# Kernel optimization log

Hardware: AMD Instinct MI355X
Metric: run time of the kernel (lower is better)

Reference implementation:

```python
import jax, jax.numpy as jnp
import numpy as np

B, D, H, NB = 16384, 1024, 256, 16

def setup_inputs() -> dict:
    key = jax.random.key(0)
    ks = jax.random.split(key, 10)
    s_d = 1.0 / np.sqrt(D)
    s_h = 1.0 / np.sqrt(H)
    return {
        "x":   jax.random.normal(ks[0], (B, D), jnp.float32),
        # switch: Linear(D,H) -> relu -> Linear(H, 3*NB)
        "Ws1": jax.random.normal(ks[1], (D, H), jnp.float32) * s_d,
        "bs1": jnp.zeros((H,), jnp.float32),
        "Ws2": jax.random.normal(ks[2], (H, 3 * NB), jnp.float32) * s_h,
        "bs2": jnp.zeros((3 * NB,), jnp.float32),
        # per-branch bottleneck FC operators: D -> H -> D
        "W1":  jax.random.normal(ks[3], (NB, D, H), jnp.float32) * s_d,
        "b1":  jnp.zeros((NB, H), jnp.float32),
        "W2":  jax.random.normal(ks[4], (NB, H, D), jnp.float32) * s_h,
        "b2":  jnp.zeros((NB, D), jnp.float32),
        # noise: uniform for gumbel, normal for reparameterized gaussian
        "u":   jax.random.uniform(ks[5], (B, NB), jnp.float32, 1e-6, 1.0 - 1e-6),
        "eps": jax.random.normal(ks[6], (B, NB), jnp.float32),
    }

def reference(x, Ws1, bs1, Ws2, bs2, W1, b1, W2, b2, u, eps):
    # switch -> control signals, reshaped to (B, 3, NB)
    ctrl = jax.nn.relu(x @ Ws1 + bs1) @ Ws2 + bs2
    ctrl = ctrl.reshape(-1, 3, NB)
    y_logits, z_mean, z_logvar = ctrl[:, 0], ctrl[:, 1], ctrl[:, 2]

    # gumbel-softmax sample (tau = 1)
    g = -jnp.log(-jnp.log(u))
    y = jax.nn.softmax(y_logits + g, axis=-1)          # soft sample (B, NB)
    y_idx = jnp.argmax(y, axis=-1)                     # hard branch per sample

    # gaussian reparameterization
    z = z_mean + jnp.exp(0.5 * z_logvar) * eps         # (B, NB)

    # per-branch bottleneck FC, z of the branch gates the bottleneck
    h = jax.nn.relu(jnp.einsum('bd,ndh->bnh', x, W1) + b1)   # (B, NB, H)
    h = h * z[:, :, None]
    o = jnp.einsum('bnh,nhd->bnd', h, W2) + b2               # (B, NB, D)

    # combine: keep only the branch selected by y_idx
    onehot = jax.nn.one_hot(y_idx, NB, dtype=x.dtype)        # (B, NB)
    out = jnp.einsum('bnd,bn->bd', o, onehot)                # (B, D)

    return (x + out, y_logits, y_idx, y, z_mean, z_logvar, z)
```

## Files before the change

### kernel.cpp

```cpp
#include <hip/hip_runtime.h>
#include <hip/hip_bf16.h>
#include <stdint.h>

#define Bn 16384
#define Dd 1024
#define Hh 256
#define NBk 16

#define O1 ((size_t)Bn*Dd)
#define O2 (O1 + (size_t)Bn*NBk)
#define O3 (O2 + (size_t)Bn)
#define O4 (O3 + (size_t)Bn*NBk)
#define O5 (O4 + (size_t)Bn*NBk)
#define O6 (O5 + (size_t)Bn*NBk)

typedef __attribute__((ext_vector_type(8))) short s16x8;
typedef __attribute__((ext_vector_type(4))) float f32x4;

#define MFMA_BF16(a,b,c) __builtin_amdgcn_mfma_f32_16x16x32_bf16((a),(b),(c),0,0,0)

__device__ __forceinline__ float blo(unsigned v){ return __uint_as_float(v << 16); }
__device__ __forceinline__ float bhi(unsigned v){ return __uint_as_float(v & 0xFFFF0000u); }
__device__ __forceinline__ unsigned short f2b(float f){
  unsigned u = __float_as_uint(f);
  return (unsigned short)((u + 0x7FFFu + ((u >> 16) & 1u)) >> 16);
}
__device__ __forceinline__ s16x8 cvt8(const f32x4 u0, const f32x4 u1) {
  s16x8 v;
  v[0]=(short)f2b(u0[0]); v[1]=(short)f2b(u0[1]); v[2]=(short)f2b(u0[2]); v[3]=(short)f2b(u0[3]);
  v[4]=(short)f2b(u1[0]); v[5]=(short)f2b(u1[1]); v[6]=(short)f2b(u1[2]); v[7]=(short)f2b(u1[3]);
  return v;
}
__device__ __forceinline__ void split8(const f32x4 u0, const f32x4 u1, s16x8& hi, s16x8& lo) {
  #pragma unroll
  for (int e = 0; e < 4; ++e) {
    const unsigned short h = f2b(u0[e]);
    hi[e] = (short)h;
    lo[e] = (short)f2b(u0[e] - __uint_as_float((unsigned)h << 16));
  }
  #pragma unroll
  for (int e = 0; e < 4; ++e) {
    const unsigned short h = f2b(u1[e]);
    hi[4+e] = (short)h;
    lo[4+e] = (short)f2b(u1[e] - __uint_as_float((unsigned)h << 16));
  }
}
__device__ __forceinline__ void gload16(const void* g, void* lds) {
  __builtin_amdgcn_global_load_lds(
      (const __attribute__((address_space(1))) unsigned int*)g,
      (__attribute__((address_space(3))) unsigned int*)lds, 16, 0, 0);
}

__global__ __launch_bounds__(256) void kA1(const float* __restrict__ x, const float* __restrict__ Ws1,
                                           const float* __restrict__ bs1, float* __restrict__ A1)
{
  const int b0 = blockIdx.x * 64;
  const int c0 = blockIdx.y * 128;
  __shared__ float XS[32][68];
  __shared__ float WS[32][128];
  const int tid = threadIdx.x;
  const int ty = tid >> 4, tx = tid & 15;
  float acc[4][8];
  #pragma unroll
  for (int r = 0; r < 4; ++r)
    #pragma unroll
    for (int c = 0; c < 8; ++c) acc[r][c] = 0.f;

  for (int k0 = 0; k0 < Dd; k0 += 32) {
    #pragma unroll
    for (int it = 0; it < 2; ++it) {
      int i = tid + 256*it;
      int row = i >> 3, kq = i & 7;
      float4 v = *(const float4*)&x[(size_t)(b0+row)*Dd + k0 + 4*kq];
      XS[4*kq+0][row] = v.x; XS[4*kq+1][row] = v.y; XS[4*kq+2][row] = v.z; XS[4*kq+3][row] = v.w;
    }
    #pragma unroll
    for (int it = 0; it < 4; ++it) {
      int i = tid + 256*it;
      int k = i >> 5, cq = i & 31;
      *(float4*)&WS[k][4*cq] = *(const float4*)&Ws1[(size_t)(k0+k)*Hh + c0 + 4*cq];
    }
    __syncthreads();
    #pragma unroll
    for (int k = 0; k < 32; ++k) {
      const float4 xv = *(const float4*)&XS[k][ty*4];
      const float4 w0 = *(const float4*)&WS[k][tx*4];
      const float4 w1 = *(const float4*)&WS[k][tx*4+64];
      const float xr[4] = {xv.x, xv.y, xv.z, xv.w};
      const float wr[8] = {w0.x,w0.y,w0.z,w0.w,w1.x,w1.y,w1.z,w1.w};
      #pragma unroll
      for (int r = 0; r < 4; ++r)
        #pragma unroll
        for (int c = 0; c < 8; ++c)
          acc[r][c] = fmaf(xr[r], wr[c], acc[r][c]);
    }
    __syncthreads();
  }
  const float4 bv0 = *(const float4*)&bs1[c0 + tx*4];
  const float4 bv1 = *(const float4*)&bs1[c0 + tx*4 + 64];
  const float br[8] = {bv0.x,bv0.y,bv0.z,bv0.w,bv1.x,bv1.y,bv1.z,bv1.w};
  #pragma unroll
  for (int r = 0; r < 4; ++r) {
    int row = b0 + ty*4 + r;
    float o[8];
    #pragma unroll
    for (int c = 0; c < 8; ++c) o[c] = fmaxf(acc[r][c] + br[c], 0.f);
    float4 s0 = {o[0],o[1],o[2],o[3]};
    float4 s1 = {o[4],o[5],o[6],o[7]};
    *(float4*)&A1[(size_t)row*Hh + c0 + tx*4]      = s0;
    *(float4*)&A1[(size_t)row*Hh + c0 + tx*4 + 64] = s1;
  }
}

__global__ __launch_bounds__(256) void kTW(const float* __restrict__ in,
                                           unsigned short* __restrict__ hi,
                                           unsigned short* __restrict__ lo)
{
  const int i0 = blockIdx.x * 32, j0 = blockIdx.y * 32;
  __shared__ float T[32][33];
  const int t = threadIdx.x;
  {
    const int ii = t >> 3, jj = (t & 7) * 4;
    float4 v = *(const float4*)&in[(size_t)(i0+ii)*Hh + j0 + jj];
    T[ii][jj] = v.x; T[ii][jj+1] = v.y; T[ii][jj+2] = v.z; T[ii][jj+3] = v.w;
  }
  __syncthreads();
  {
    const int jo = t >> 3, io = (t & 7) * 4;
    ushort4 sh, sl;
    float v0 = T[io+0][jo], v1 = T[io+1][jo], v2 = T[io+2][jo], v3 = T[io+3][jo];
    unsigned short h;
    h = f2b(v0); sh.x = h; sl.x = f2b(v0 - __uint_as_float((unsigned)h << 16));
    h = f2b(v1); sh.y = h; sl.y = f2b(v1 - __uint_as_float((unsigned)h << 16));
    h = f2b(v2); sh.z = h; sl.z = f2b(v2 - __uint_as_float((unsigned)h << 16));
    h = f2b(v3); sh.w = h; sl.w = f2b(v3 - __uint_as_float((unsigned)h << 16));
    *(ushort4*)&hi[(size_t)(j0+jo)*Dd + i0 + io] = sh;
    *(ushort4*)&lo[(size_t)(j0+jo)*Dd + i0 + io] = sl;
  }
}

__global__ __launch_bounds__(256) void kT2(const float* __restrict__ Ws2, float* __restrict__ Ws2T)
{
  const int j = blockIdx.x;
  const int k = threadIdx.x;
  Ws2T[(size_t)j * Hh + k] = Ws2[(size_t)k * 48 + j];
}

__global__ __launch_bounds__(256) void kA1s3(const float* __restrict__ x,
    const unsigned short* __restrict__ Whi, const unsigned short* __restrict__ Wlo,
    const float* __restrict__ bs1, float* __restrict__ A1)
{
  __shared__ __align__(16) unsigned short Xh[32*64];
  __shared__ __align__(16) unsigned short Xl[32*64];
  __shared__ __align__(16) unsigned short Bh[128*64];
  __shared__ __align__(16) unsigned short Bl[128*64];

  const int bid = blockIdx.x;
  const int b0 = (bid >> 1) * 32;
  const int cb = bid & 1;
  const int tid = threadIdx.x, l = tid & 63, w = tid >> 6;

  const int xrow = tid >> 3, xga = tid & 7;
  const int xdst = xrow * 128 + (xga ^ (xrow & 7)) * 16;
  const size_t xsrc = (size_t)(b0 + xrow) * Dd + xga * 8;

  const unsigned short *hsrc[4], *lsrc[4];
  const unsigned short* Hbase = Whi + (size_t)(cb * 128) * Dd;
  const unsigned short* Lbase = Wlo + (size_t)(cb * 128) * Dd;
  #pragma unroll
  for (int t = 0; t < 4; ++t) {
    const int col = (w * 4 + t) * 8 + (l >> 3);
    const int sa = (l & 7) ^ (col & 7);
    hsrc[t] = Hbase + (size_t)col * Dd + sa * 8;
    lsrc[t] = Lbase + (size_t)col * Dd + sa * 8;
  }

  f32x4 acc[2][2];
  #pragma unroll
  for (int a = 0; a < 2; ++a)
    #pragma unroll
    for (int b_ = 0; b_ < 2; ++b_)
      #pragma unroll
      for (int e = 0; e < 4; ++e) acc[a][b_][e] = 0.f;

  f32x4 xa = *(const f32x4*)&x[xsrc];
  f32x4 xb = *(const f32x4*)&x[xsrc + 4];

  for (int kc = 0; kc < 16; ++kc) {
    #pragma unroll
    for (int t = 0; t < 4; ++t) {
      gload16(hsrc[t] + kc * 64, (char*)Bh + (w * 4 + t) * 1024);
      gload16(lsrc[t] + kc * 64, (char*)Bl + (w * 4 + t) * 1024);
    }
    {
      s16x8 hi8, lo8;
      split8(xa, xb, hi8, lo8);
      *(s16x8*)((char*)Xh + xdst) = hi8;
      *(s16x8*)((char*)Xl + xdst) = lo8;
    }
    __syncthreads();

    if (kc < 15) {
      xa = *(const f32x4*)&x[xsrc + (kc + 1) * 64];
      xb = *(const f32x4*)&x[xsrc + (kc + 1) * 64 + 4];
    }

    #pragma unroll
    for (int kk = 0; kk < 2; ++kk) {
      s16x8 ah[2], al[2], bh[2], bl[2];
      #pragma unroll
      for (int rf = 0; rf < 2; ++rf) {
        const int row = rf * 16 + (l & 15);
        const int g = (kk * 4 + (l >> 4)) ^ (row & 7);
        ah[rf] = *(const s16x8*)((const char*)Xh + row * 128 + g * 16);
        al[rf] = *(const s16x8*)((const char*)Xl + row * 128 + g * 16);
      }
      #pragma unroll
      for (int cf = 0; cf < 2; ++cf) {
        const int col = w * 32 + cf * 16 + (l & 15);
        const int g = (kk * 4 + (l >> 4)) ^ (col & 7);
        bh[cf] = *(const s16x8*)((const char*)Bh + col * 128 + g * 16);
        bl[cf] = *(const s16x8*)((const char*)Bl + col * 128 + g * 16);
      }
      #pragma unroll
      for (int rf = 0; rf < 2; ++rf)
        #pragma unroll
        for (int cf = 0; cf < 2; ++cf) {
          acc[rf][cf] = MFMA_BF16(ah[rf], bh[cf], acc[rf][cf]);
          acc[rf][cf] = MFMA_BF16(ah[rf], bl[cf], acc[rf][cf]);
          acc[rf][cf] = MFMA_BF16(al[rf], bh[cf], acc[rf][cf]);
        }
    }
    __syncthreads();
  }

  #pragma unroll
  for (int rf = 0; rf < 2; ++rf)
    #pragma unroll
    for (int cf = 0; cf < 2; ++cf)
      #pragma unroll
      for (int rg = 0; rg < 4; ++rg) {
        const int row = b0 + rf * 16 + (l >> 4) * 4 + rg;
        const int col = cb * 128 + w * 32 + cf * 16 + (l & 15);
        A1[(size_t)row * Hh + col] = fmaxf(acc[rf][cf][rg] + bs1[col], 0.f);
      }
}

__global__ __launch_bounds__(256) void kA2(const float* __restrict__ Ws2, const float* __restrict__ bs2,
                                           float* out)
{
  const int b0 = blockIdx.x * 64;
  __shared__ float XS[32][68];
  __shared__ float WC[32][48];
  const int tid = threadIdx.x;
  const int rg = tid >> 4, jg = tid & 15;
  float acc[4][3];
  #pragma unroll
  for (int r = 0; r < 4; ++r) { acc[r][0]=0.f; acc[r][1]=0.f; acc[r][2]=0.f; }
  const float* A1 = out;
  for (int kc = 0; kc < 8; ++kc) {
    const int k0 = kc*32;
    #pragma unroll
    for (int it = 0; it < 2; ++it) {
      int i = tid + 256*it;
      int row = i >> 3, kq = i & 7;
      float4 v = *(const float4*)&A1[(size_t)(b0+row)*Hh + k0 + 4*kq];
      XS[4*kq+0][row]=v.x; XS[4*kq+1][row]=v.y; XS[4*kq+2][row]=v.z; XS[4*kq+3][row]=v.w;
    }
    #pragma unroll
    for (int it = 0; it < 2; ++it) {
      int i = tid + 256*it;
      if (i < 384) {
        int k = i / 12, jq = i % 12;
        *(float4*)&WC[k][4*jq] = *(const float4*)&Ws2[(size_t)(k0+k)*48 + 4*jq];
      }
    }
    __syncthreads();
    #pragma unroll
    for (int k = 0; k < 32; ++k) {
      const float4 av = *(const float4*)&XS[k][rg*4];
      const float ar[4] = {av.x,av.y,av.z,av.w};
      const float w0 = WC[k][jg], w1 = WC[k][jg+16], w2 = WC[k][jg+32];
      #pragma unroll
      for (int r = 0; r < 4; ++r) {
        acc[r][0] = fmaf(ar[r], w0, acc[r][0]);
        acc[r][1] = fmaf(ar[r], w1, acc[r][1]);
        acc[r][2] = fmaf(ar[r], w2, acc[r][2]);
      }
    }
    __syncthreads();
  }
  const float c0b = bs2[jg], c1b = bs2[jg+16], c2b = bs2[jg+32];
  #pragma unroll
  for (int r = 0; r < 4; ++r) {
    size_t row = (size_t)b0 + rg*4 + r;
    out[O1 + row*NBk + jg] = acc[r][0] + c0b;
    out[O4 + row*NBk + jg] = acc[r][1] + c1b;
    out[O5 + row*NBk + jg] = acc[r][2] + c2b;
  }
}

__global__ __launch_bounds__(256) void kB2(const float* __restrict__ u, const float* __restrict__ eps,
                                           float* out, int* __restrict__ idxw, float* __restrict__ zsel,
                                           int* __restrict__ counts)
{
  const int e = blockIdx.x * 256 + threadIdx.x;
  const int b = e >> 4, j = e & 15;
  const float yl = out[O1 + e];
  const float zm = out[O4 + e];
  const float zv = out[O5 + e];
  const float s  = yl - logf(-logf(u[e]));
  const float z  = zm + expf(0.5f * zv) * eps[e];

  float bv = s; int bj = j;
  #pragma unroll
  for (int m = 8; m >= 1; m >>= 1) {
    const float ov = __shfl_xor(bv, m, 16);
    const int   oj = __shfl_xor(bj, m, 16);
    if (ov > bv || (ov == bv && oj < bj)) { bv = ov; bj = oj; }
  }
  const float ex = expf(s - bv);
  float sum = ex;
  #pragma unroll
  for (int m = 8; m >= 1; m >>= 1) sum += __shfl_xor(sum, m, 16);
  const float inv = 1.f / sum;

  out[O3 + e] = ex * inv;
  out[O6 + e] = z;
  if (j == bj) {
    out[O2 + b] = (float)bj;
    idxw[b] = bj;
    zsel[b] = z;
    atomicAdd(&counts[bj], 1);
  }
}

__global__ __launch_bounds__(256) void kB3(const float* __restrict__ A1, const float* __restrict__ Ws2T,
                                           const float* __restrict__ bs2,
                                           const float* __restrict__ u, const float* __restrict__ eps,
                                           float* out, int* __restrict__ idxw, float* __restrict__ zsel)
{
  __shared__ float AS[16][258];
  __shared__ float WS[48][258];
  const int tid = threadIdx.x;
  const int brow0 = blockIdx.x * 16;

  #pragma unroll
  for (int it = 0; it < 4; ++it) {
    const int i = tid + 256 * it;
    const int row = i >> 6, kq = i & 63;
    const f32x4 v = *(const f32x4*)&A1[(size_t)(brow0 + row) * Hh + kq * 4];
    *(f32x4*)&AS[row][kq * 4] = v;
  }
  #pragma unroll
  for (int it = 0; it < 12; ++it) {
    const int i = tid + 256 * it;
    const int row = i >> 6, kq = i & 63;
    const f32x4 v = *(const f32x4*)&Ws2T[(size_t)row * Hh + kq * 4];
    *(f32x4*)&WS[row][kq * 4] = v;
  }
  __syncthreads();

  const int e = blockIdx.x * 256 + tid;
  const int b = e >> 4, j = tid & 15;
  const int rl = tid >> 4;

  float c0 = 0.f, c1 = 0.f, c2 = 0.f;
  #pragma unroll 4
  for (int k = 0; k < Hh; k += 4) {
    const f32x4 av = *(const f32x4*)&AS[rl][k];
    const f32x4 wa = *(const f32x4*)&WS[j][k];
    const f32x4 wb = *(const f32x4*)&WS[j + 16][k];
    const f32x4 wc = *(const f32x4*)&WS[j + 32][k];
    #pragma unroll
    for (int kk = 0; kk < 4; ++kk) {
      c0 = fmaf(av[kk], wa[kk], c0);
      c1 = fmaf(av[kk], wb[kk], c1);
      c2 = fmaf(av[kk], wc[kk], c2);
    }
  }
  const float yl = c0 + bs2[j];
  const float zm = c1 + bs2[j + 16];
  const float zv = c2 + bs2[j + 32];

  const float s = yl - logf(-logf(u[e]));
  const float z = zm + expf(0.5f * zv) * eps[e];

  float bv = s; int bj = j;
  #pragma unroll
  for (int m = 8; m >= 1; m >>= 1) {
    const float ov = __shfl_xor(bv, m, 16);
    const int   oj = __shfl_xor(bj, m, 16);
    if (ov > bv || (ov == bv && oj < bj)) { bv = ov; bj = oj; }
  }
  const float ex = expf(s - bv);
  float sum = ex;
  #pragma unroll
  for (int m = 8; m >= 1; m >>= 1) sum += __shfl_xor(sum, m, 16);
  const float inv = 1.f / sum;

  out[O1 + e] = yl;
  out[O4 + e] = zm;
  out[O5 + e] = zv;
  out[O3 + e] = ex * inv;
  out[O6 + e] = z;
  if (j == bj) {
    out[O2 + b] = (float)bj;
    idxw[b] = bj;
    zsel[b] = z;
  }
}

__global__ __launch_bounds__(256) void kH(const int* __restrict__ idxw, int* __restrict__ counts)
{
  __shared__ int lh[NBk];
  const int tid = threadIdx.x;
  if (tid < NBk) lh[tid] = 0;
  __syncthreads();
  atomicAdd(&lh[idxw[blockIdx.x * 256 + tid]], 1);
  __syncthreads();
  if (tid < NBk && lh[tid]) atomicAdd(&counts[tid], lh[tid]);
}

__global__ void kP(const int* __restrict__ counts, int* __restrict__ offs, int* __restrict__ cursor,
                   int* __restrict__ bpre, int* __restrict__ tp1, int* __restrict__ tp2,
                   int* __restrict__ seg)
{
  if (threadIdx.x == 0 && blockIdx.x == 0) {
    int a = 0, bb = 0, t1 = 0, t2 = 0, sg = 0;
    for (int n = 0; n < NBk; ++n) {
      offs[n] = a; cursor[n] = a; bpre[n] = bb; tp1[n] = t1; tp2[n] = t2; seg[n] = sg;
      const int c = counts[n];
      a  += c;
      bb += (c + 31) >> 5;
      t1 += (c + 63) >> 6;
      t2 += (c + 127) >> 7;
      sg += ((c + 127) >> 7) * 128;
    }
    offs[NBk] = a; bpre[NBk] = bb; tp1[NBk] = t1; tp2[NBk] = t2; seg[NBk] = sg;
  }
}

__global__ __launch_bounds__(256) void kS(const int* __restrict__ idxw, int* __restrict__ cursor,
                                          int* __restrict__ rowlist)
{
  const int b = blockIdx.x * 256 + threadIdx.x;
  const int n = idxw[b];
  const int pos = atomicAdd(&cursor[n], 1);
  rowlist[pos] = b;
}

__global__ __launch_bounds__(256) void kS2(const int* __restrict__ idxw, int* __restrict__ cursor,
                                           int* __restrict__ rowlist)
{
  __shared__ int lh[NBk];
  __shared__ int gb[NBk];
  const int tid = threadIdx.x;
  const int b = blockIdx.x * 256 + tid;
  const int n = idxw[b];
  if (tid < NBk) lh[tid] = 0;
  __syncthreads();
  const int rank = atomicAdd(&lh[n], 1);
  __syncthreads();
  if (tid < NBk) gb[tid] = lh[tid] ? atomicAdd(&cursor[tid], lh[tid]) : 0;
  __syncthreads();
  rowlist[gb[n] + rank] = b;
}

__global__ __launch_bounds__(256) void kT(const float* __restrict__ in, unsigned short* __restrict__ out,
                                          int R, int C)
{
  const int n = blockIdx.z;
  in  += (size_t)n * R * C;
  out += (size_t)n * R * C;
  const int i0 = blockIdx.x * 32, j0 = blockIdx.y * 32;
  __shared__ float T[32][33];
  const int t = threadIdx.x;
  {
    const int ii = t >> 3, jj = (t & 7) * 4;
    float4 v = *(const float4*)&in[(size_t)(i0+ii)*C + j0 + jj];
    T[ii][jj] = v.x; T[ii][jj+1] = v.y; T[ii][jj+2] = v.z; T[ii][jj+3] = v.w;
  }
  __syncthreads();
  {
    const int jo = t >> 3, io = (t & 7) * 4;
    ushort4 st;
    st.x = f2b(T[io+0][jo]);
    st.y = f2b(T[io+1][jo]);
    st.z = f2b(T[io+2][jo]);
    st.w = f2b(T[io+3][jo]);
    *(ushort4*)&out[(size_t)(j0+jo)*R + i0 + io] = st;
  }
}

__global__ __launch_bounds__(256) void kG1(const float* __restrict__ x,
    const unsigned short* __restrict__ W1T, const float* __restrict__ b1,
    const int* __restrict__ rowlist, const float* __restrict__ zsel,
    const int* __restrict__ offs, const int* __restrict__ tp1, const int* __restrict__ seg,
    unsigned short* __restrict__ hbuf)
{
  __shared__ __align__(16) float Xs[64*64];
  __shared__ __align__(16) unsigned short Wsh[128*64];
  __shared__ int rows_s[64];
  __shared__ float zrs[64];

  const int bid = blockIdx.x;
  const int tile = bid >> 1, cb = bid & 1;
  if (tile >= tp1[NBk]) return;
  int n = 0;
  while (tile >= tp1[n+1]) ++n;
  const int tt = tile - tp1[n];
  const int base = offs[n], cnt = offs[n+1] - base;
  const int r0 = tt * 64;
  const int tid = threadIdx.x, l = tid & 63, w = tid >> 6;
  const int wr = w >> 1, wc = w & 1;

  if (tid < 64) {
    int r = r0 + tid;
    int g = rowlist[base + (r < cnt ? r : cnt - 1)];
    rows_s[tid] = g;
    zrs[tid] = zsel[g];
  }
  __syncthreads();

  size_t xsrc[4];
  const unsigned short* wsrc[4];
  const unsigned short* Wbase = W1T + (size_t)n * (Hh * Dd) + (size_t)(cb * 128) * Dd;
  #pragma unroll
  for (int t = 0; t < 4; ++t) {
    {
      int row = (w * 4 + t) * 4 + (l >> 4);
      int ga = (l & 15) ^ (row & 7);
      xsrc[t] = (size_t)rows_s[row] * Dd + ga * 4;
    }
    {
      int row = (w * 4 + t) * 8 + (l >> 3);
      int sa = (l & 7) ^ (row & 7);
      wsrc[t] = Wbase + (size_t)row * Dd + sa * 8;
    }
  }

  f32x4 acc[2][4];
  #pragma unroll
  for (int a = 0; a < 2; ++a)
    #pragma unroll
    for (int b_ = 0; b_ < 4; ++b_)
      #pragma unroll
      for (int e = 0; e < 4; ++e) acc[a][b_][e] = 0.f;

  for (int kc = 0; kc < 16; ++kc) {
    #pragma unroll
    for (int t = 0; t < 4; ++t) {
      gload16(&x[xsrc[t] + kc * 64], (char*)Xs + (w * 4 + t) * 1024);
      gload16(wsrc[t] + kc * 64, (char*)Wsh + (w * 4 + t) * 1024);
    }
    __syncthreads();

    #pragma unroll
    for (int kk = 0; kk < 2; ++kk) {
      s16x8 af[2], bf[4];
      #pragma unroll
      for (int rf = 0; rf < 2; ++rf) {
        const int row = wr * 32 + rf * 16 + (l & 15);
        const int gl = 8 * kk + 2 * (l >> 4);
        const int g0 = gl ^ (row & 7), g1 = (gl + 1) ^ (row & 7);
        f32x4 u0 = *(const f32x4*)((const char*)Xs + row * 256 + g0 * 16);
        f32x4 u1 = *(const f32x4*)((const char*)Xs + row * 256 + g1 * 16);
        af[rf] = cvt8(u0, u1);
      }
      #pragma unroll
      for (int cf = 0; cf < 4; ++cf) {
        const int col = wc * 64 + cf * 16 + (l & 15);
        const int s8 = (4 * kk + (l >> 4)) ^ (col & 7);
        bf[cf] = *(const s16x8*)((const char*)Wsh + col * 128 + s8 * 16);
      }
      #pragma unroll
      for (int rf = 0; rf < 2; ++rf)
        #pragma unroll
        for (int cf = 0; cf < 4; ++cf)
          acc[rf][cf] = MFMA_BF16(af[rf], bf[cf], acc[rf][cf]);
    }
    __syncthreads();
  }

  const size_t hrow0 = (size_t)seg[n] + r0;
  #pragma unroll
  for (int rf = 0; rf < 2; ++rf)
    #pragma unroll
    for (int cf = 0; cf < 4; ++cf)
      #pragma unroll
      for (int rg = 0; rg < 4; ++rg) {
        const int rloc = wr * 32 + rf * 16 + (l >> 4) * 4 + rg;
        const int col = cb * 128 + wc * 64 + cf * 16 + (l & 15);
        const float hv = fmaxf(acc[rf][cf][rg] + b1[n * Hh + col], 0.f) * zrs[rloc];
        hbuf[(hrow0 + rloc) * Hh + col] = f2b(hv);
      }
}

__global__ __launch_bounds__(256) void kG2(const float* __restrict__ x,
    const unsigned short* __restrict__ W2T, const float* __restrict__ b2,
    const unsigned short* __restrict__ hbuf, const int* __restrict__ rowlist,
    const int* __restrict__ offs, const int* __restrict__ tp2, const int* __restrict__ seg,
    float* __restrict__ out)
{
  __shared__ __align__(16) unsigned short As[128*64];
  __shared__ __align__(16) unsigned short Bs[128*64];
  __shared__ int rows_s[128];

  const int bid = blockIdx.x;
  const int tile = bid >> 3, cb = bid & 7;
  if (tile >= tp2[NBk]) return;
  int n = 0;
  while (tile >= tp2[n+1]) ++n;
  const int tt = tile - tp2[n];
  const int base = offs[n], cnt = offs[n+1] - base;
  const int r0 = tt * 128;
  const int tid = threadIdx.x, l = tid & 63, w = tid >> 6;
  const int wr = w >> 1, wc = w & 1;

  if (tid < 128) {
    int r = r0 + tid;
    rows_s[tid] = rowlist[base + (r < cnt ? r : cnt - 1)];
  }
  __syncthreads();

  const unsigned short* Abase = hbuf + (size_t)(seg[n] + r0) * Hh;
  const unsigned short* Bbase = W2T + (size_t)n * (Hh * Dd) + (size_t)(cb * 128) * Hh;

  const unsigned short* asrc[4];
  const unsigned short* bsrc[4];
  #pragma unroll
  for (int t = 0; t < 4; ++t) {
    const int row = (w * 4 + t) * 8 + (l >> 3);
    const int sa = (l & 7) ^ (row & 7);
    asrc[t] = Abase + (size_t)row * Hh + sa * 8;
    bsrc[t] = Bbase + (size_t)row * Hh + sa * 8;
  }

  f32x4 acc[4][4];
  #pragma unroll
  for (int a = 0; a < 4; ++a)
    #pragma unroll
    for (int b_ = 0; b_ < 4; ++b_)
      #pragma unroll
      for (int e = 0; e < 4; ++e) acc[a][b_][e] = 0.f;

  for (int kc = 0; kc < 4; ++kc) {
    #pragma unroll
    for (int t = 0; t < 4; ++t) {
      gload16(asrc[t] + kc * 64, (char*)As + (w * 4 + t) * 1024);
      gload16(bsrc[t] + kc * 64, (char*)Bs + (w * 4 + t) * 1024);
    }
    __syncthreads();

    #pragma unroll
    for (int kk = 0; kk < 2; ++kk) {
      s16x8 af[4], bf[4];
      #pragma unroll
      for (int rf = 0; rf < 4; ++rf) {
        const int row = wr * 64 + rf * 16 + (l & 15);
        const int s8 = (4 * kk + (l >> 4)) ^ (row & 7);
        af[rf] = *(const s16x8*)((const char*)As + row * 128 + s8 * 16);
      }
      #pragma unroll
      for (int cf = 0; cf < 4; ++cf) {
        const int col = wc * 64 + cf * 16 + (l & 15);
        const int s8 = (4 * kk + (l >> 4)) ^ (col & 7);
        bf[cf] = *(const s16x8*)((const char*)Bs + col * 128 + s8 * 16);
      }
      #pragma unroll
      for (int rf = 0; rf < 4; ++rf)
        #pragma unroll
        for (int cf = 0; cf < 4; ++cf)
          acc[rf][cf] = MFMA_BF16(af[rf], bf[cf], acc[rf][cf]);
    }
    __syncthreads();
  }

  #pragma unroll
  for (int rf = 0; rf < 4; ++rf)
    #pragma unroll
    for (int rg = 0; rg < 4; ++rg) {
      const int rloc = wr * 64 + rf * 16 + (l >> 4) * 4 + rg;
      if (r0 + rloc < cnt) {
        const int g = rows_s[rloc];
        #pragma unroll
        for (int cf = 0; cf < 4; ++cf) {
          const int col = cb * 128 + wc * 64 + cf * 16 + (l & 15);
          out[(size_t)g * Dd + col] = acc[rf][cf][rg] + b2[n * Dd + col] + x[(size_t)g * Dd + col];
        }
      }
    }
}

extern "C" void kernel_launch(void* const* d_in, const int* in_sizes, int n_in,
                              void* d_out, int out_size, void* d_ws, size_t ws_size,
                              hipStream_t stream) {
  const float* x   = (const float*)d_in[0];
  const float* Ws1 = (const float*)d_in[1];
  const float* bs1 = (const float*)d_in[2];
  const float* Ws2 = (const float*)d_in[3];
  const float* bs2 = (const float*)d_in[4];
  const float* W1  = (const float*)d_in[5];
  const float* b1  = (const float*)d_in[6];
  const float* W2  = (const float*)d_in[7];
  const float* b2  = (const float*)d_in[8];
  const float* u   = (const float*)d_in[9];
  const float* eps = (const float*)d_in[10];
  float* out = (float*)d_out;

  char* ws = (char*)d_ws;
  int*   counts  = (int*)(ws + 0);
  int*   cursor  = (int*)(ws + 64);
  int*   bpre    = (int*)(ws + 128);
  int*   offs    = (int*)(ws + 256);
  int*   tp1     = (int*)(ws + 384);
  int*   tp2     = (int*)(ws + 512);
  int*   seg     = (int*)(ws + 640);
  int*   idxw    = (int*)(ws + 4096);
  float* zsel    = (float*)(ws + 4096 + 65536);
  int*   rowlist = (int*)(ws + 4096 + 131072);
  float* Ws2T    = (float*)(ws + 786432);
  unsigned short* W1T  = (unsigned short*)(ws + ((size_t)1 << 20));
  unsigned short* W2T  = (unsigned short*)(ws + ((size_t)9 << 20));
  unsigned short* hbuf = (unsigned short*)(ws + ((size_t)17 << 20));
  unsigned short* Whi  = (unsigned short*)(ws + ((size_t)27 << 20));
  unsigned short* Wlo  = (unsigned short*)(ws + ((size_t)27 << 20) + (512<<10));

  const bool f2 = ws_size >= ((size_t)28 << 20);
  const bool f1 = ws_size >= ((size_t)18 << 20);

  hipMemsetAsync(d_ws, 0, 4096, stream);
  if (f1 || f2) {
    kT<<<dim3(32, 8, 16), 256, 0, stream>>>(W1, W1T, Dd, Hh);
    kT<<<dim3(8, 32, 16), 256, 0, stream>>>(W2, W2T, Hh, Dd);
  }
  if (f2) {
    kTW<<<dim3(32, 8), 256, 0, stream>>>(Ws1, Whi, Wlo);
    kT2<<<dim3(48), 256, 0, stream>>>(Ws2, Ws2T);
    kA1s3<<<dim3(1024), 256, 0, stream>>>(x, Whi, Wlo, bs1, out);
    kB3<<<dim3(Bn/16), 256, 0, stream>>>(out, Ws2T, bs2, u, eps, out, idxw, zsel);
    kH <<<dim3(Bn/256), 256, 0, stream>>>(idxw, counts);
  } else {
    kA1<<<dim3(Bn/64, 2), 256, 0, stream>>>(x, Ws1, bs1, out);
    kA2<<<dim3(Bn/64), 256, 0, stream>>>(Ws2, bs2, out);
    kB2<<<dim3(Bn*NBk/256), 256, 0, stream>>>(u, eps, out, idxw, zsel, counts);
  }
  kP <<<dim3(1), 64, 0, stream>>>(counts, offs, cursor, bpre, tp1, tp2, seg);
  if (f2) {
    kS2<<<dim3(Bn/256), 256, 0, stream>>>(idxw, cursor, rowlist);
    kG1<<<dim3(544), 256, 0, stream>>>(x, W1T, b1, rowlist, zsel, offs, tp1, seg, hbuf);
    kG2<<<dim3(1152), 256, 0, stream>>>(x, W2T, b2, hbuf, rowlist, offs, tp2, seg, out);
  } else {
    kS<<<dim3(Bn/256), 256, 0, stream>>>(idxw, cursor, rowlist);
  }
}
```

Before: 160.1 us.

## Double-buffer shared memory in switch GEMM kernel to overlap loads with MFMA

Converts the first switch-layer GEMM kernel to a double-buffered LDS scheme in dynamic shared memory. The next k-chunk of split hi/lo weights and x is staged while MFMAs run on the current chunk, with one barrier per iteration instead of two. LDS per block grows to 80KB, which lowers how many blocks fit on a CU and may need a large dynamic shared-memory allocation to launch.

New measurement: 169.2 us. +5.7%, slower.

```diff
diff --git a/kernel.cpp b/kernel.cpp
--- a/kernel.cpp
+++ b/kernel.cpp
@@ -146,14 +146,11 @@
   Ws2T[(size_t)j * Hh + k] = Ws2[(size_t)k * 48 + j];
 }
 
-__global__ __launch_bounds__(256) void kA1s3(const float* __restrict__ x,
+__global__ __launch_bounds__(256) void kA1s4(const float* __restrict__ x,
     const unsigned short* __restrict__ Whi, const unsigned short* __restrict__ Wlo,
     const float* __restrict__ bs1, float* __restrict__ A1)
 {
-  __shared__ __align__(16) unsigned short Xh[32*64];
-  __shared__ __align__(16) unsigned short Xl[32*64];
-  __shared__ __align__(16) unsigned short Bh[128*64];
-  __shared__ __align__(16) unsigned short Bl[128*64];
+  extern __shared__ __align__(16) char sm[];
 
   const int bid = blockIdx.x;
   const int b0 = (bid >> 1) * 32;
@@ -161,7 +158,7 @@
   const int tid = threadIdx.x, l = tid & 63, w = tid >> 6;
 
   const int xrow = tid >> 3, xga = tid & 7;
-  const int xdst = xrow * 128 + (xga ^ (xrow & 7)) * 16;
+  const int xdst = xrow * 128 + ((xga ^ (xrow & 7)) * 16);
   const size_t xsrc = (size_t)(b0 + xrow) * Dd + xga * 8;
 
   const unsigned short *hsrc[4], *lsrc[4];
@@ -185,24 +182,43 @@
 
   f32x4 xa = *(const f32x4*)&x[xsrc];
   f32x4 xb = *(const f32x4*)&x[xsrc + 4];
+  #pragma unroll
+  for (int t = 0; t < 4; ++t) {
+    gload16(hsrc[t], sm + 16384 + (w * 4 + t) * 1024);
+    gload16(lsrc[t], sm + 16384 + 16384 + (w * 4 + t) * 1024);
+  }
+  {
+    s16x8 hi8, lo8;
+    split8(xa, xb, hi8, lo8);
+    *(s16x8*)(sm + xdst) = hi8;
+    *(s16x8*)(sm + 4096 + xdst) = lo8;
+  }
+  xa = *(const f32x4*)&x[xsrc + 64];
+  xb = *(const f32x4*)&x[xsrc + 68];
+  __syncthreads();
 
   for (int kc = 0; kc < 16; ++kc) {
-    #pragma unroll
-    for (int t = 0; t < 4; ++t) {
-      gload16(hsrc[t] + kc * 64, (char*)Bh + (w * 4 + t) * 1024);
-      gload16(lsrc[t] + kc * 64, (char*)Bl + (w * 4 + t) * 1024);
-    }
-    {
-      s16x8 hi8, lo8;
-      split8(xa, xb, hi8, lo8);
-      *(s16x8*)((char*)Xh + xdst) = hi8;
-      *(s16x8*)((char*)Xl + xdst) = lo8;
-    }
-    __syncthreads();
+    const char* Xb = sm + (kc & 1) * 8192;
+    const char* Bb = sm + 16384 + (kc & 1) * 32768;
 
     if (kc < 15) {
-      xa = *(const f32x4*)&x[xsrc + (kc + 1) * 64];
-      xb = *(const f32x4*)&x[xsrc + (kc + 1) * 64 + 4];
+      const int nb = (kc + 1) & 1;
+      char* Bn_ = sm + 16384 + nb * 32768;
+      #pragma unroll
+      for (int t = 0; t < 4; ++t) {
+        gload16(hsrc[t] + (kc + 1) * 64, Bn_ + (w * 4 + t) * 1024);
+        gload16(lsrc[t] + (kc + 1) * 64, Bn_ + 16384 + (w * 4 + t) * 1024);
+      }
+      {
+        s16x8 hi8, lo8;
+        split8(xa, xb, hi8, lo8);
+        *(s16x8*)(sm + nb * 8192 + xdst) = hi8;
+        *(s16x8*)(sm + nb * 8192 + 4096 + xdst) = lo8;
+      }
+      if (kc < 14) {
+        xa = *(const f32x4*)&x[xsrc + (kc + 2) * 64];
+        xb = *(const f32x4*)&x[xsrc + (kc + 2) * 64 + 4];
+      }
     }
 
     #pragma unroll
@@ -212,15 +228,15 @@
       for (int rf = 0; rf < 2; ++rf) {
         const int row = rf * 16 + (l & 15);
         const int g = (kk * 4 + (l >> 4)) ^ (row & 7);
-        ah[rf] = *(const s16x8*)((const char*)Xh + row * 128 + g * 16);
-        al[rf] = *(const s16x8*)((const char*)Xl + row * 128 + g * 16);
+        ah[rf] = *(const s16x8*)(Xb + row * 128 + g * 16);
+        al[rf] = *(const s16x8*)(Xb + 4096 + row * 128 + g * 16);
       }
       #pragma unroll
       for (int cf = 0; cf < 2; ++cf) {
         const int col = w * 32 + cf * 16 + (l & 15);
         const int g = (kk * 4 + (l >> 4)) ^ (col & 7);
-        bh[cf] = *(const s16x8*)((const char*)Bh + col * 128 + g * 16);
-        bl[cf] = *(const s16x8*)((const char*)Bl + col * 128 + g * 16);
+        bh[cf] = *(const s16x8*)(Bb + col * 128 + g * 16);
+        bl[cf] = *(const s16x8*)(Bb + 16384 + col * 128 + g * 16);
       }
       #pragma unroll
       for (int rf = 0; rf < 2; ++rf)
@@ -738,7 +754,7 @@
   if (f2) {
     kTW<<<dim3(32, 8), 256, 0, stream>>>(Ws1, Whi, Wlo);
     kT2<<<dim3(48), 256, 0, stream>>>(Ws2, Ws2T);
-    kA1s3<<<dim3(1024), 256, 0, stream>>>(x, Whi, Wlo, bs1, out);
+    kA1s4<<<dim3(1024), 256, 81920, stream>>>(x, Whi, Wlo, bs1, out);
     kB3<<<dim3(Bn/16), 256, 0, stream>>>(out, Ws2T, bs2, u, eps, out, idxw, zsel);
     kH <<<dim3(Bn/256), 256, 0, stream>>>(idxw, counts);
   } else {
```

## Enlarge switch GEMM tile to 64 rows and load fp32 x via async copies

Applied to the files above, without the earlier changes.

The first switch GEMM kernel now processes 64 batch rows per block instead of 32, with a 2x2 warp layout where each warp computes a 32x64 output tile. This halves the grid and doubles reuse of each loaded weight tile. The x tile is now copied as fp32 straight into shared memory with direct global-to-LDS loads, and the bf16 hi/lo split moves to the point where fragments are read. This removes the register prefetch and the shared-memory store of pre-split values. The cost is a repeated split per warp, more shared memory and more accumulator registers, which may lower occupancy.

New measurement: 159.8 us, median of 2. No clear change (-0.2%).

```diff
diff --git a/kernel.cpp b/kernel.cpp
--- a/kernel.cpp
+++ b/kernel.cpp
@@ -146,89 +146,82 @@
   Ws2T[(size_t)j * Hh + k] = Ws2[(size_t)k * 48 + j];
 }
 
-__global__ __launch_bounds__(256) void kA1s3(const float* __restrict__ x,
+__global__ __launch_bounds__(256) void kA1s(const float* __restrict__ x,
     const unsigned short* __restrict__ Whi, const unsigned short* __restrict__ Wlo,
     const float* __restrict__ bs1, float* __restrict__ A1)
 {
-  __shared__ __align__(16) unsigned short Xh[32*64];
-  __shared__ __align__(16) unsigned short Xl[32*64];
+  __shared__ __align__(16) float Xs[64*64];
   __shared__ __align__(16) unsigned short Bh[128*64];
   __shared__ __align__(16) unsigned short Bl[128*64];
 
   const int bid = blockIdx.x;
-  const int b0 = (bid >> 1) * 32;
+  const int b0 = (bid >> 1) * 64;
   const int cb = bid & 1;
   const int tid = threadIdx.x, l = tid & 63, w = tid >> 6;
-
-  const int xrow = tid >> 3, xga = tid & 7;
-  const int xdst = xrow * 128 + (xga ^ (xrow & 7)) * 16;
-  const size_t xsrc = (size_t)(b0 + xrow) * Dd + xga * 8;
-
+  const int wr = w >> 1, wc = w & 1;
+
+  size_t xsrc[4];
   const unsigned short *hsrc[4], *lsrc[4];
   const unsigned short* Hbase = Whi + (size_t)(cb * 128) * Dd;
   const unsigned short* Lbase = Wlo + (size_t)(cb * 128) * Dd;
   #pragma unroll
   for (int t = 0; t < 4; ++t) {
-    const int col = (w * 4 + t) * 8 + (l >> 3);
-    const int sa = (l & 7) ^ (col & 7);
-    hsrc[t] = Hbase + (size_t)col * Dd + sa * 8;
-    lsrc[t] = Lbase + (size_t)col * Dd + sa * 8;
-  }
-
-  f32x4 acc[2][2];
+    {
+      int row = (w * 4 + t) * 4 + (l >> 4);
+      int ga = (l & 15) ^ (row & 7);
+      xsrc[t] = (size_t)(b0 + row) * Dd + ga * 4;
+    }
+    {
+      int row = (w * 4 + t) * 8 + (l >> 3);
+      int sa = (l & 7) ^ (row & 7);
+      hsrc[t] = Hbase + (size_t)row * Dd + sa * 8;
+      lsrc[t] = Lbase + (size_t)row * Dd + sa * 8;
+    }
+  }
+
+  f32x4 acc[2][4];
   #pragma unroll
   for (int a = 0; a < 2; ++a)
     #pragma unroll
-    for (int b_ = 0; b_ < 2; ++b_)
+    for (int b_ = 0; b_ < 4; ++b_)
       #pragma unroll
       for (int e = 0; e < 4; ++e) acc[a][b_][e] = 0.f;
 
-  f32x4 xa = *(const f32x4*)&x[xsrc];
-  f32x4 xb = *(const f32x4*)&x[xsrc + 4];
-
   for (int kc = 0; kc < 16; ++kc) {
     #pragma unroll
     for (int t = 0; t < 4; ++t) {
+      gload16(&x[xsrc[t] + kc * 64], (char*)Xs + (w * 4 + t) * 1024);
       gload16(hsrc[t] + kc * 64, (char*)Bh + (w * 4 + t) * 1024);
       gload16(lsrc[t] + kc * 64, (char*)Bl + (w * 4 + t) * 1024);
     }
-    {
-      s16x8 hi8, lo8;
-      split8(xa, xb, hi8, lo8);
-      *(s16x8*)((char*)Xh + xdst) = hi8;
-      *(s16x8*)((char*)Xl + xdst) = lo8;
-    }
-    __syncthreads();
-
-    if (kc < 15) {
-      xa = *(const f32x4*)&x[xsrc + (kc + 1) * 64];
-      xb = *(const f32x4*)&x[xsrc + (kc + 1) * 64 + 4];
-    }
+    __syncthreads();
 
     #pragma unroll
     for (int kk = 0; kk < 2; ++kk) {
-      s16x8 ah[2], al[2], bh[2], bl[2];
+      s16x8 ahi[2], alo[2], bh[4], bl[4];
       #pragma unroll
       for (int rf = 0; rf < 2; ++rf) {
-        const int row = rf * 16 + (l & 15);
-        const int g = (kk * 4 + (l >> 4)) ^ (row & 7);
-        ah[rf] = *(const s16x8*)((const char*)Xh + row * 128 + g * 16);
-        al[rf] = *(const s16x8*)((const char*)Xl + row * 128 + g * 16);
-      }
-      #pragma unroll
-      for (int cf = 0; cf < 2; ++cf) {
-        const int col = w * 32 + cf * 16 + (l & 15);
-        const int g = (kk * 4 + (l >> 4)) ^ (col & 7);
-        bh[cf] = *(const s16x8*)((const char*)Bh + col * 128 + g * 16);
-        bl[cf] = *(const s16x8*)((const char*)Bl + col * 128 + g * 16);
+        const int row = wr * 32 + rf * 16 + (l & 15);
+        const int gl = 8 * kk + 2 * (l >> 4);
+        const int g0 = gl ^ (row & 7), g1 = (gl + 1) ^ (row & 7);
+        f32x4 u0 = *(const f32x4*)((const char*)Xs + row * 256 + g0 * 16);
+        f32x4 u1 = *(const f32x4*)((const char*)Xs + row * 256 + g1 * 16);
+        split8(u0, u1, ahi[rf], alo[rf]);
+      }
+      #pragma unroll
+      for (int cf = 0; cf < 4; ++cf) {
+        const int col = wc * 64 + cf * 16 + (l & 15);
+        const int s8 = (4 * kk + (l >> 4)) ^ (col & 7);
+        bh[cf] = *(const s16x8*)((const char*)Bh + col * 128 + s8 * 16);
+        bl[cf] = *(const s16x8*)((const char*)Bl + col * 128 + s8 * 16);
       }
       #pragma unroll
       for (int rf = 0; rf < 2; ++rf)
         #pragma unroll
-        for (int cf = 0; cf < 2; ++cf) {
-          acc[rf][cf] = MFMA_BF16(ah[rf], bh[cf], acc[rf][cf]);
-          acc[rf][cf] = MFMA_BF16(ah[rf], bl[cf], acc[rf][cf]);
-          acc[rf][cf] = MFMA_BF16(al[rf], bh[cf], acc[rf][cf]);
+        for (int cf = 0; cf < 4; ++cf) {
+          acc[rf][cf] = MFMA_BF16(ahi[rf], bh[cf], acc[rf][cf]);
+          acc[rf][cf] = MFMA_BF16(ahi[rf], bl[cf], acc[rf][cf]);
+          acc[rf][cf] = MFMA_BF16(alo[rf], bh[cf], acc[rf][cf]);
         }
     }
     __syncthreads();
@@ -237,11 +230,11 @@
   #pragma unroll
   for (int rf = 0; rf < 2; ++rf)
     #pragma unroll
-    for (int cf = 0; cf < 2; ++cf)
+    for (int cf = 0; cf < 4; ++cf)
       #pragma unroll
       for (int rg = 0; rg < 4; ++rg) {
-        const int row = b0 + rf * 16 + (l >> 4) * 4 + rg;
-        const int col = cb * 128 + w * 32 + cf * 16 + (l & 15);
+        const int row = b0 + wr * 32 + rf * 16 + (l >> 4) * 4 + rg;
+        const int col = cb * 128 + wc * 64 + cf * 16 + (l & 15);
         A1[(size_t)row * Hh + col] = fmaxf(acc[rf][cf][rg] + bs1[col], 0.f);
       }
 }
@@ -738,7 +731,7 @@
   if (f2) {
     kTW<<<dim3(32, 8), 256, 0, stream>>>(Ws1, Whi, Wlo);
     kT2<<<dim3(48), 256, 0, stream>>>(Ws2, Ws2T);
-    kA1s3<<<dim3(1024), 256, 0, stream>>>(x, Whi, Wlo, bs1, out);
+    kA1s<<<dim3(512), 256, 0, stream>>>(x, Whi, Wlo, bs1, out);
     kB3<<<dim3(Bn/16), 256, 0, stream>>>(out, Ws2T, bs2, u, eps, out, idxw, zsel);
     kH <<<dim3(Bn/256), 256, 0, stream>>>(idxw, counts);
   } else {
```
